# Kernel optimization log

Measured on AMD Instinct MI355X. Metric: run time of the kernel, lower is better.

Reference implementation:

```python
import jax, jax.numpy as jnp
import numpy as np

IN_F = 512
OUT_F = 512
TREES = 50
DEPTH = 10  # levels above leaves; 2^DEPTH leaves per tree


def _build_forest(T, D):
    """Forest of T perfect binary trees. Nodes laid out level-by-level (leaves first).
    Returns node_order [N], adjacency [E,2] (parent, child; children consecutive,
    left then right, edges sorted by parent), edge_order [E]."""
    per = 2 ** (D + 1) - 1
    no = np.zeros(per, np.int64)
    adj_parts, eo_parts = [], []
    start, prev = 0, None
    for l in range(D + 1):
        n_l = 2 ** (D - l)
        idx = np.arange(start, start + n_l, dtype=np.int64)
        no[idx] = l
        if l > 0:
            parents = np.repeat(idx, 2)          # each parent twice
            adj_parts.append(np.stack([parents, prev], 1))  # prev = 2*n_l children, pairs consecutive
            eo_parts.append(np.full(2 * n_l, l, np.int64))
        prev, start = idx, start + n_l
    adj = np.concatenate(adj_parts, 0)
    eo = np.concatenate(eo_parts, 0)
    offs = np.arange(T, dtype=np.int64) * per
    node_order = np.tile(no, T)
    adjacency = (adj[None] + offs[:, None, None]).reshape(-1, 2)
    edge_order = np.tile(eo, T)
    return node_order, adjacency, edge_order


def setup_inputs() -> dict:
    key = jax.random.key(0)
    ks = jax.random.split(key, 8)
    no, adj, eo = _build_forest(TREES, DEPTH)
    N = no.shape[0]
    s_in = 1.0 / np.sqrt(IN_F).astype(np.float32)
    s_h = 1.0 / np.sqrt(OUT_F).astype(np.float32)
    return {
        "features": jax.random.normal(ks[0], (N, IN_F), jnp.float32),
        "node_order": jnp.asarray(no),
        "adjacency_list": jnp.asarray(adj),
        "edge_order": jnp.asarray(eo),
        "W_iou_w": jax.random.normal(ks[1], (3 * OUT_F, IN_F), jnp.float32) * s_in,
        "W_iou_b": jax.random.normal(ks[2], (3 * OUT_F,), jnp.float32) * s_in,
        "U_iou_l": jax.random.normal(ks[3], (3 * OUT_F, OUT_F), jnp.float32) * s_h,
        "U_iou_r": jax.random.normal(ks[4], (3 * OUT_F, OUT_F), jnp.float32) * s_h,
        "W_f_w": jax.random.normal(ks[5], (OUT_F, IN_F), jnp.float32) * s_in,
        "W_f_b": jax.random.normal(ks[6], (OUT_F,), jnp.float32) * s_in,
        "U_f_l": jax.random.normal(ks[7], (OUT_F, OUT_F), jnp.float32) * s_h,
        "U_f_r": jax.random.normal(jax.random.fold_in(key, 99), (OUT_F, OUT_F), jnp.float32) * s_h,
    }


def reference(features, node_order, adjacency_list, edge_order,
              W_iou_w, W_iou_b, U_iou_l, U_iou_r, W_f_w, W_f_b, U_f_l, U_f_r):
    # Tree topology is static integer data: hoist it to numpy so per-level index
    # sets are concrete (the original torch code host-syncs the same way).
    no = np.asarray(node_order)
    ao = np.asarray(adjacency_list)
    eo = np.asarray(edge_order)
    N, H = features.shape[0], W_f_w.shape[0]
    h = jnp.zeros((N, H), features.dtype)
    c = jnp.zeros((N, H), features.dtype)
    for l in range(int(no.max()) + 1):
        nodes = jnp.asarray(np.nonzero(no == l)[0])   # parents at this level, sorted
        x = features[nodes]                            # [P, F]
        if l == 0:
            iou = x @ W_iou_w.T + W_iou_b
            i, o, u = jnp.split(iou, 3, axis=1)
            c_new = jax.nn.sigmoid(i) * jnp.tanh(u)
        else:
            e = ao[eo == l]                            # [2P, 2]; children consecutive per parent
            p_rep = jnp.asarray(e[:, 0])               # parent repeated per child
            children = jnp.asarray(e[:, 1])
            ch = h[children]                           # [2P, H]
            cc = c[children]                           # [2P, H]
            iou = (x @ W_iou_w.T + W_iou_b
                   + ch[0::2] @ U_iou_l.T              # left child h
                   + ch[1::2] @ U_iou_r.T)             # right child h
            i, o, u = jnp.split(iou, 3, axis=1)
            wf = features[p_rep] @ W_f_w.T + W_f_b     # [2P, H]
            f_l = jax.nn.sigmoid(wf + ch @ U_f_l.T)
            f_r = jax.nn.sigmoid(wf + ch @ U_f_r.T)
            fc = (f_l + f_r) * cc                      # [2P, H]
            c_new = jax.nn.sigmoid(i) * jnp.tanh(u) + fc.reshape(-1, 2, H).sum(1)
        h_new = jax.nn.sigmoid(o) * jnp.tanh(c_new)
        c = c.at[nodes].set(c_new)
        h = h.at[nodes].set(h_new)
    return h, c
```

## Files before the change

kernel.cpp:

```cpp
#include <hip/hip_runtime.h>
#include <hip/hip_bf16.h>

#define TREES_ 50
#define PER_ 2047
#define NN_ (TREES_ * PER_)
#define NINT_ (TREES_ * 1023)
#define NLEAF_ (TREES_ * 1024)

typedef __attribute__((ext_vector_type(8))) short s8v;
typedef __attribute__((ext_vector_type(4))) float f4v;

__device__ __forceinline__ unsigned short f2bf(float f) {
  union { float f; unsigned u; } v; v.f = f;
  unsigned r = v.u + 0x7FFFu + ((v.u >> 16) & 1u);
  return (unsigned short)(r >> 16);
}
__device__ __forceinline__ float bf2f(unsigned short s) {
  union { unsigned u; float f; } v; v.u = ((unsigned)s) << 16;
  return v.f;
}
__device__ __forceinline__ float sigm(float x) { return 1.f / (1.f + __expf(-x)); }
__device__ __forceinline__ float tanh_s(float x) {
  float ax = fabsf(x);
  float e = __expf(2.f * ax);
  float t = 1.f - 2.f / (e + 1.f);
  return copysignf(t, x);
}
__device__ __forceinline__ f4v fz4() { f4v z; z[0]=0.f; z[1]=0.f; z[2]=0.f; z[3]=0.f; return z; }

#if defined(__has_builtin)
#if __has_builtin(__builtin_amdgcn_global_load_lds)
#define HAS_GLD 1
#endif
#endif
__device__ __forceinline__ void gld16(const void* g, void* l) {
#ifdef HAS_GLD
  __builtin_amdgcn_global_load_lds(
      (const __attribute__((address_space(1))) unsigned int*)g,
      (__attribute__((address_space(3))) unsigned int*)l, 16, 0, 0);
#else
  *(s8v*)l = *(const s8v*)g;
#endif
}

__device__ __forceinline__ int xcd_swz(int bid, int nwg) {
  int q = nwg >> 3, r = nwg & 7, x = bid & 7, pos = bid >> 3;
  int base = (x < r) ? x * (q + 1) : r * (q + 1) + (x - r) * q;
  return base + pos;
}

#define LDS_BYTE(row, c16) ((row) * 128 + (((c16) ^ ((row) & 7)) << 4))

#define MFMA_STEP(Ap, Bp)                                                     \
  _Pragma("unroll") for (int kk = 0; kk < 2; ++kk) {                          \
    s8v af[4], bf_[4];                                                        \
    _Pragma("unroll") for (int i = 0; i < 4; ++i) {                           \
      int R = wr * 64 + i * 16 + lr;                                          \
      af[i] = *(const s8v*)((const char*)(Ap) + LDS_BYTE(R, kk * 4 + lg));    \
    }                                                                         \
    _Pragma("unroll") for (int j = 0; j < 4; ++j) {                           \
      int R = wc * 64 + j * 16 + lr;                                          \
      bf_[j] = *(const s8v*)((const char*)(Bp) + LDS_BYTE(R, kk * 4 + lg));   \
    }                                                                         \
    _Pragma("unroll") for (int i = 0; i < 4; ++i)                             \
      _Pragma("unroll") for (int j = 0; j < 4; ++j)                           \
        acc[i][j] = __builtin_amdgcn_mfma_f32_16x16x32_bf16(af[i], bf_[j],    \
                                                            acc[i][j], 0, 0, 0); \
  }

#define VMCNT8() asm volatile("s_waitcnt vmcnt(8)" ::: "memory")
#define VMCNT0() asm volatile("s_waitcnt vmcnt(0)" ::: "memory")
#define LGKM0()  asm volatile("s_waitcnt lgkmcnt(0)" ::: "memory")
#define SBAR()   __builtin_amdgcn_s_barrier()
#define SCHEDB() __builtin_amdgcn_sched_barrier(0)

#define PIPELINE(STAGEM, NT)                                       \
  STAGEM(0, 0)                                                     \
  STAGEM(1, 64)                                                    \
  {                                                                \
    int cur = 0;                                                   \
    for (int t = 0; t < (NT) - 1; ++t) {                           \
      VMCNT8(); SBAR();                                            \
      __builtin_amdgcn_s_setprio(1);                               \
      MFMA_STEP(AsB + cur * 8192, BsB + cur * 8192)                \
      __builtin_amdgcn_s_setprio(0);                               \
      LGKM0(); SCHEDB(); SBAR();                                   \
      if (t + 2 < (NT)) { STAGEM(cur, (t + 2) * 64) }              \
      cur ^= 1;                                                    \
    }                                                              \
    VMCNT0(); SBAR();                                              \
    MFMA_STEP(AsB + cur * 8192, BsB + cur * 8192)                  \
  }

__global__ __launch_bounds__(256) void feat2bf(const float* __restrict__ feat,
                                               unsigned short* __restrict__ FB) {
  long long i = (long long)blockIdx.x * 256 + threadIdx.x;
  if (i >= (long long)NN_ * 64) return;
  const float* src = feat + i * 8;
  float4 f0 = *(const float4*)src;
  float4 f1 = *(const float4*)(src + 4);
  s8v v;
  v[0] = (short)f2bf(f0.x); v[1] = (short)f2bf(f0.y);
  v[2] = (short)f2bf(f0.z); v[3] = (short)f2bf(f0.w);
  v[4] = (short)f2bf(f1.x); v[5] = (short)f2bf(f1.y);
  v[6] = (short)f2bf(f1.z); v[7] = (short)f2bf(f1.w);
  *(s8v*)(FB + i * 8) = v;
}

__global__ __launch_bounds__(256) void prep_weights(
    const float* __restrict__ Wiou, const float* __restrict__ Ul,
    const float* __restrict__ Ur,  const float* __restrict__ Wf,
    const float* __restrict__ Ufl, const float* __restrict__ Ufr,
    unsigned short* __restrict__ UCAT2, unsigned short* __restrict__ UFLR,
    unsigned short* __restrict__ WFB) {
  int i = blockIdx.x * 256 + threadIdx.x;
  if (i < 1536 * 1536) {
    int r = i / 1536, c = i - r * 1536;
    float v = (c < 512) ? Ul[r * 512 + c]
            : (c < 1024) ? Ur[r * 512 + (c - 512)]
                         : Wiou[r * 512 + (c - 1024)];
    UCAT2[i] = f2bf(v);
  }
  if (i < 1024 * 512) {
    int r = i >> 9, k = i & 511;
    int c = r >> 1, s = r & 1;
    UFLR[i] = f2bf(s ? Ufr[c * 512 + k] : Ufl[c * 512 + k]);
  }
  if (i < 512 * 512) WFB[i] = f2bf(Wf[i]);
}

__global__ __launch_bounds__(256) void pre_mm(
    const unsigned short* __restrict__ FB, const unsigned short* __restrict__ WFB,
    const unsigned short* __restrict__ UCAT2,
    const float* __restrict__ bfb, const float* __restrict__ biou,
    unsigned short* __restrict__ WF, unsigned short* __restrict__ LIOU,
    int nwgW, int nwgL) {
  __shared__ __align__(16) unsigned short AsB[2 * 128 * 64];
  __shared__ __align__(16) unsigned short BsB[2 * 128 * 64];
  const int tid = threadIdx.x;
  const int wid = tid >> 6, lane = tid & 63;
  const int wr = wid >> 1, wc = wid & 1;
  const int lr = lane & 15, lg = lane >> 4;
  f4v acc[4][4];
#pragma unroll
  for (int i = 0; i < 4; ++i)
#pragma unroll
    for (int j = 0; j < 4; ++j) acc[i][j] = fz4();

  const unsigned short* aA[4]; const unsigned short* aB[4];
  int tm, tn;
  const bool isW = (int)blockIdx.x < nwgW;
  if (isW) {
    const int swz = xcd_swz(blockIdx.x, nwgW);
    tn = swz & 3; tm = swz >> 2;
#pragma unroll
    for (int L = 0; L < 4; ++L) {
      int q = L * 256 + tid;
      int row = q >> 3, c16g = (q & 7) ^ (row & 7);
      int m = tm * 128 + row; if (m >= NINT_) m = NINT_ - 1;
      unsigned t = (unsigned)m / 1023u;
      int node = (int)t * 2047 + 1024 + (m - (int)t * 1023);
      aA[L] = FB + (size_t)node * 512 + c16g * 8;
      int n = tn * 128 + row;
      aB[L] = WFB + (size_t)n * 512 + c16g * 8;
    }
  } else {
    const int swz = xcd_swz((int)blockIdx.x - nwgW, nwgL);
    tn = swz % 12; tm = swz / 12;
#pragma unroll
    for (int L = 0; L < 4; ++L) {
      int q = L * 256 + tid;
      int row = q >> 3, c16g = (q & 7) ^ (row & 7);
      int m = tm * 128 + row;
      int node = (m >> 10) * 2047 + (m & 1023);
      aA[L] = FB + (size_t)node * 512 + c16g * 8;
      int n = tn * 128 + row;
      aB[L] = UCAT2 + (size_t)n * 1536 + 1024 + c16g * 8;
    }
  }
#define STAGE_P(bb, kofs)                                         \
  _Pragma("unroll") for (int L = 0; L < 4; ++L) {                 \
    int q = L * 256 + tid;                                        \
    gld16(aA[L] + (kofs), AsB + (bb) * 8192 + q * 8);             \
    gld16(aB[L] + (kofs), BsB + (bb) * 8192 + q * 8);             \
  }
  PIPELINE(STAGE_P, 8)

  if (isW) {
#pragma unroll
    for (int i = 0; i < 4; ++i)
#pragma unroll
      for (int j = 0; j < 4; ++j) {
        int n = tn * 128 + wc * 64 + j * 16 + lr;
        float bias = bfb[n];
#pragma unroll
        for (int r = 0; r < 4; ++r) {
          int m = tm * 128 + wr * 64 + i * 16 + lg * 4 + r;
          if (m < NINT_) WF[(size_t)m * 512 + n] = f2bf(acc[i][j][r] + bias);
        }
      }
  } else {
#pragma unroll
    for (int i = 0; i < 4; ++i)
#pragma unroll
      for (int j = 0; j < 4; ++j) {
        int n = tn * 128 + wc * 64 + j * 16 + lr;
        float bias = biou[n];
#pragma unroll
        for (int r = 0; r < 4; ++r) {
          int m = tm * 128 + wr * 64 + i * 16 + lg * 4 + r;
          LIOU[(size_t)m * 1536 + n] = f2bf(acc[i][j][r] + bias);
        }
      }
  }
}

__global__ __launch_bounds__(256) void leaf_ew(
    const unsigned short* __restrict__ LIOU,
    float* __restrict__ h_out, float* __restrict__ c_out,
    unsigned short* __restrict__ HB) {
  int idx = blockIdx.x * 256 + threadIdx.x;
  int r = idx >> 7;
  int c4 = (idx & 127) << 2;
  int g = (r >> 10) * 2047 + (r & 1023);
  const unsigned short* pr = LIOU + (size_t)r * 1536;
  ushort4 iv = *(const ushort4*)(pr + c4);
  ushort4 ov = *(const ushort4*)(pr + 512 + c4);
  ushort4 uv = *(const ushort4*)(pr + 1024 + c4);
  float4 hv, cv; ushort4 hb;
  float cc, hh;
  cc = sigm(bf2f(iv.x)) * tanh_s(bf2f(uv.x)); hh = sigm(bf2f(ov.x)) * tanh_s(cc);
  cv.x = cc; hv.x = hh; hb.x = f2bf(hh);
  cc = sigm(bf2f(iv.y)) * tanh_s(bf2f(uv.y)); hh = sigm(bf2f(ov.y)) * tanh_s(cc);
  cv.y = cc; hv.y = hh; hb.y = f2bf(hh);
  cc = sigm(bf2f(iv.z)) * tanh_s(bf2f(uv.z)); hh = sigm(bf2f(ov.z)) * tanh_s(cc);
  cv.z = cc; hv.z = hh; hb.z = f2bf(hh);
  cc = sigm(bf2f(iv.w)) * tanh_s(bf2f(uv.w)); hh = sigm(bf2f(ov.w)) * tanh_s(cc);
  cv.w = cc; hv.w = hh; hb.w = f2bf(hh);
  *(float4*)(h_out + (size_t)g * 512 + c4) = hv;
  *(float4*)(c_out + (size_t)g * 512 + c4) = cv;
  *(ushort4*)(HB + (size_t)g * 512 + c4) = hb;
}

__global__ __launch_bounds__(256) void lvl_gemm(
    const unsigned short* __restrict__ HB, const unsigned short* __restrict__ FB,
    const unsigned short* __restrict__ UFLR, const unsigned short* __restrict__ UCAT2,
    const unsigned short* __restrict__ WF, const float* __restrict__ biou,
    const float* __restrict__ c_out, float* __restrict__ h_out,
    unsigned short* __restrict__ IOU,
    int P, int shift, int start_l, int start_lm1, int nwg1, int nwg2) {
  __shared__ __align__(16) unsigned short AsB[2 * 128 * 64];
  __shared__ __align__(16) unsigned short BsB[2 * 128 * 64];
  const int tid = threadIdx.x;
  const int wid = tid >> 6, lane = tid & 63;
  const int wr = wid >> 1, wc = wid & 1;
  const int lr = lane & 15, lg = lane >> 4;
  const int pmask = (1 << shift) - 1;
  f4v acc[4][4];
#pragma unroll
  for (int i = 0; i < 4; ++i)
#pragma unroll
    for (int j = 0; j < 4; ++j) acc[i][j] = fz4();

  if ((int)blockIdx.x < nwg1) {
    const int swz = xcd_swz(blockIdx.x, nwg1);
    const int tn = swz & 7, tm = swz >> 3;
    const int M2 = 2 * P;
    const int cmask = (2 << shift) - 1;
    const unsigned short* aA[4]; const unsigned short* aB[4];
#pragma unroll
    for (int L = 0; L < 4; ++L) {
      int q = L * 256 + tid;
      int row = q >> 3, c16g = (q & 7) ^ (row & 7);
      int jg = tm * 128 + row; if (jg >= M2) jg = M2 - 1;
      int t = jg >> (shift + 1), idx = jg & cmask;
      aA[L] = HB + (size_t)(t * PER_ + start_lm1 + idx) * 512 + c16g * 8;
      int n = tn * 128 + row;
      aB[L] = UFLR + (size_t)n * 512 + c16g * 8;
    }
#define STAGE_G1(bb, kofs)                                        \
  _Pragma("unroll") for (int L = 0; L < 4; ++L) {                 \
    int q = L * 256 + tid;                                        \
    gld16(aA[L] + (kofs), AsB + (bb) * 8192 + q * 8);             \
    gld16(aB[L] + (kofs), BsB + (bb) * 8192 + q * 8);             \
  }
    PIPELINE(STAGE_G1, 8)

    const int soff = start_l - 1024;
#pragma unroll
    for (int i = 0; i < 4; ++i) {
      int mbase = tm * 128 + wr * 64 + i * 16;
#pragma unroll
      for (int j = 0; j < 4; ++j) {
        int nn = tn * 128 + wc * 64 + j * 16 + lr;
        int hcol = nn >> 1;
        float fc[4];
#pragma unroll
        for (int r = 0; r < 4; ++r) {
          int m = mbase + lg * 4 + r;
          int mm = (m < M2) ? m : 0;
          int pidx = mm >> 1;
          int t = pidx >> shift, k = pidx & pmask;
          float wf = bf2f(WF[(size_t)(t * 1023 + soff + k) * 512 + hcol]);
          float sv = sigm(wf + acc[i][j][r]);
          float spair = sv + __shfl_xor(sv, 1, 64);
          float cc = 0.f;
          if ((lr & 1) == 0)
            cc = c_out[(size_t)(t * PER_ + start_lm1 + (mm & cmask)) * 512 + hcol];
          fc[r] = spair * cc;
        }
        if ((lr & 1) == 0) {
          int p0 = (mbase >> 1) + lg * 2;
          if (p0 < P) {
            int t0 = p0 >> shift, k0p = p0 & pmask;
            h_out[(size_t)(t0 * PER_ + start_l + k0p) * 512 + hcol] = fc[0] + fc[1];
          }
          int p1 = (mbase >> 1) + lg * 2 + 1;
          if (p1 < P) {
            int t1 = p1 >> shift, k1p = p1 & pmask;
            h_out[(size_t)(t1 * PER_ + start_l + k1p) * 512 + hcol] = fc[2] + fc[3];
          }
        }
      }
    }
  } else {
    const int swz = xcd_swz((int)blockIdx.x - nwg1, nwg2);
    const int tn = swz % 12, tm = swz / 12;
    const unsigned short* aHB[4]; const unsigned short* aFB[4];
    const unsigned short* aB[4];
#pragma unroll
    for (int L = 0; L < 4; ++L) {
      int q = L * 256 + tid;
      int row = q >> 3, c16g = (q & 7) ^ (row & 7);
      int p = tm * 128 + row; if (p >= P) p = P - 1;
      int t = p >> shift, kp = p & pmask;
      aHB[L] = HB + (size_t)(t * PER_ + start_lm1) * 512 + (size_t)kp * 1024 + c16g * 8;
      aFB[L] = FB + (size_t)(t * PER_ + start_l + kp) * 512 + c16g * 8 - 1024;
      int n = tn * 128 + row;
      aB[L] = UCAT2 + (size_t)n * 1536 + c16g * 8;
    }
#define STAGE_G2(bb, kofs)                                                    \
  _Pragma("unroll") for (int L = 0; L < 4; ++L) {                             \
    int q = L * 256 + tid;                                                    \
    const unsigned short* srcA =                                              \
        ((kofs) < 1024) ? aHB[L] + (kofs) : aFB[L] + (kofs);                  \
    gld16(srcA, AsB + (bb) * 8192 + q * 8);                                   \
    gld16(aB[L] + (kofs), BsB + (bb) * 8192 + q * 8);                         \
  }
    PIPELINE(STAGE_G2, 24)
#pragma unroll
    for (int i = 0; i < 4; ++i)
#pragma unroll
      for (int j = 0; j < 4; ++j) {
        int n = tn * 128 + wc * 64 + j * 16 + lr;
        float bias = biou[n];
#pragma unroll
        for (int r = 0; r < 4; ++r) {
          int m = tm * 128 + wr * 64 + i * 16 + lg * 4 + r;
          if (m < P) IOU[(size_t)m * 1536 + n] = f2bf(acc[i][j][r] + bias);
        }
      }
  }
}

__global__ __launch_bounds__(256) void g3_kernel(
    const unsigned short* __restrict__ IOU,
    float* __restrict__ h_out, float* __restrict__ c_out,
    unsigned short* __restrict__ HB, int P, int shift, int start_l) {
  int idx = blockIdx.x * 256 + threadIdx.x;
  int p = idx >> 7;
  if (p >= P) return;
  int c4 = (idx & 127) << 2;
  int t = p >> shift, k = p & ((1 << shift) - 1);
  size_t pg = (size_t)(t * PER_ + start_l + k);
  const unsigned short* ir = IOU + (size_t)p * 1536;
  ushort4 iv = *(const ushort4*)(ir + c4);
  ushort4 ov = *(const ushort4*)(ir + 512 + c4);
  ushort4 uv = *(const ushort4*)(ir + 1024 + c4);
  float4 fcs = *(const float4*)(h_out + pg * 512 + c4);
  float4 hv, cv; ushort4 hb;
  float cc, hh;
  cc = sigm(bf2f(iv.x)) * tanh_s(bf2f(uv.x)) + fcs.x; hh = sigm(bf2f(ov.x)) * tanh_s(cc);
  cv.x = cc; hv.x = hh; hb.x = f2bf(hh);
  cc = sigm(bf2f(iv.y)) * tanh_s(bf2f(uv.y)) + fcs.y; hh = sigm(bf2f(ov.y)) * tanh_s(cc);
  cv.y = cc; hv.y = hh; hb.y = f2bf(hh);
  cc = sigm(bf2f(iv.z)) * tanh_s(bf2f(uv.z)) + fcs.z; hh = sigm(bf2f(ov.z)) * tanh_s(cc);
  cv.z = cc; hv.z = hh; hb.z = f2bf(hh);
  cc = sigm(bf2f(iv.w)) * tanh_s(bf2f(uv.w)) + fcs.w; hh = sigm(bf2f(ov.w)) * tanh_s(cc);
  cv.w = cc; hv.w = hh; hb.w = f2bf(hh);
  *(float4*)(h_out + pg * 512 + c4) = hv;
  *(float4*)(c_out + pg * 512 + c4) = cv;
  *(ushort4*)(HB + pg * 512 + c4) = hb;
}

__global__ void fill_sentinel(float* out, int n) {
  int i = blockIdx.x * 256 + threadIdx.x;
  if (i < n) out[i] = 12345.0f;
}

extern "C" void kernel_launch(void* const* d_in, const int* in_sizes, int n_in,
                              void* d_out, int out_size, void* d_ws, size_t ws_size,
                              hipStream_t stream) {
  (void)in_sizes; (void)n_in; (void)out_size;
  const float* feat = (const float*)d_in[0];
  const float* Wiou = (const float*)d_in[4];
  const float* biou = (const float*)d_in[5];
  const float* Ul   = (const float*)d_in[6];
  const float* Ur   = (const float*)d_in[7];
  const float* Wf   = (const float*)d_in[8];
  const float* bfb  = (const float*)d_in[9];
  const float* Ufl  = (const float*)d_in[10];
  const float* Ufr  = (const float*)d_in[11];
  float* h_out = (float*)d_out;
  float* c_out = h_out + (size_t)NN_ * 512;

  const size_t OFF_HB   = 0;
  const size_t SZ_HB    = (size_t)NN_ * 512 * 2;
  const size_t OFF_FB   = OFF_HB + SZ_HB;
  const size_t SZ_FB    = (size_t)NN_ * 512 * 2;
  const size_t OFF_WFm  = OFF_FB + SZ_FB;
  const size_t SZ_WF    = (size_t)NINT_ * 512 * 2;
  const size_t OFF_UC2  = OFF_WFm + SZ_WF;
  const size_t SZ_UC2   = 1536 * 1536 * 2;
  const size_t OFF_UFLR = OFF_UC2 + SZ_UC2;
  const size_t SZ_UFLR  = 1024 * 512 * 2;
  const size_t OFF_WFB  = OFF_UFLR + SZ_UFLR;
  const size_t SZ_WFB   = 512 * 512 * 2;
  const size_t OFF_LIOU = OFF_WFB + SZ_WFB;
  const size_t SZ_LIOU  = (size_t)NLEAF_ * 1536 * 2;
  const size_t NEEDED   = OFF_LIOU + SZ_LIOU;

  if (ws_size < NEEDED) {
    int n = 2 * NN_ * 512;
    fill_sentinel<<<(n + 255) / 256, 256, 0, stream>>>((float*)d_out, n);
    return;
  }

  char* ws = (char*)d_ws;
  unsigned short* HB    = (unsigned short*)(ws + OFF_HB);
  unsigned short* FB    = (unsigned short*)(ws + OFF_FB);
  unsigned short* WF    = (unsigned short*)(ws + OFF_WFm);
  unsigned short* UCAT2 = (unsigned short*)(ws + OFF_UC2);
  unsigned short* UFLR  = (unsigned short*)(ws + OFF_UFLR);
  unsigned short* WFB   = (unsigned short*)(ws + OFF_WFB);
  unsigned short* LIOU  = (unsigned short*)(ws + OFF_LIOU);
  unsigned short* IOU   = (unsigned short*)(ws + OFF_LIOU);

  prep_weights<<<9216, 256, 0, stream>>>(Wiou, Ul, Ur, Wf, Ufl, Ufr,
                                         UCAT2, UFLR, WFB);
  feat2bf<<<(NN_ * 64 + 255) / 256, 256, 0, stream>>>(feat, FB);
  {
    int nwgW = ((NINT_ + 127) / 128) * 4;
    int nwgL = (NLEAF_ / 128) * 12;
    pre_mm<<<nwgW + nwgL, 256, 0, stream>>>(FB, WFB, UCAT2, bfb, biou,
                                            WF, LIOU, nwgW, nwgL);
  }
  leaf_ew<<<(NLEAF_ * 128) / 256, 256, 0, stream>>>(LIOU, h_out, c_out, HB);

  for (int l = 1; l <= 10; ++l) {
    int shift = 10 - l;
    int P = TREES_ << shift;
    int start_l   = 2048 - (1 << (11 - l));
    int start_lm1 = 2048 - (1 << (12 - l));
    int nwg1 = ((2 * P + 127) / 128) * 8;
    int nwg2 = ((P + 127) / 128) * 12;
    lvl_gemm<<<nwg1 + nwg2, 256, 0, stream>>>(HB, FB, UFLR, UCAT2, WF, biou,
                                              c_out, h_out, IOU,
                                              P, shift, start_l, start_lm1,
                                              nwg1, nwg2);
    int g3b = (P * 128 + 255) / 256;
    g3_kernel<<<g3b, 256, 0, stream>>>(IOU, h_out, c_out, HB, P, shift, start_l);
  }
}
```

Before: 1.460 ms.

## Fuse leaf IOU GEMM with leaf elementwise gates, drop LIOU buffer

```diff
diff --git a/kernel.cpp b/kernel.cpp
--- a/kernel.cpp
+++ b/kernel.cpp
@@ -129,117 +129,126 @@
   if (i < 512 * 512) WFB[i] = f2bf(Wf[i]);
 }
 
-__global__ __launch_bounds__(256) void pre_mm(
+__global__ __launch_bounds__(256) void wf_gemm(
     const unsigned short* __restrict__ FB, const unsigned short* __restrict__ WFB,
-    const unsigned short* __restrict__ UCAT2,
-    const float* __restrict__ bfb, const float* __restrict__ biou,
-    unsigned short* __restrict__ WF, unsigned short* __restrict__ LIOU,
-    int nwgW, int nwgL) {
+    const float* __restrict__ bfb, unsigned short* __restrict__ WF, int nwg) {
   __shared__ __align__(16) unsigned short AsB[2 * 128 * 64];
   __shared__ __align__(16) unsigned short BsB[2 * 128 * 64];
   const int tid = threadIdx.x;
+  const int swz = xcd_swz(blockIdx.x, nwg);
+  const int tn = swz & 3, tm = swz >> 2;
   const int wid = tid >> 6, lane = tid & 63;
   const int wr = wid >> 1, wc = wid & 1;
   const int lr = lane & 15, lg = lane >> 4;
+  const unsigned short* aA[4]; const unsigned short* aB[4];
+#pragma unroll
+  for (int L = 0; L < 4; ++L) {
+    int q = L * 256 + tid;
+    int row = q >> 3, c16g = (q & 7) ^ (row & 7);
+    int m = tm * 128 + row; if (m >= NINT_) m = NINT_ - 1;
+    int t = (int)((unsigned)m / 1023u);
+    int node = t * 2047 + 1024 + (m - t * 1023);
+    aA[L] = FB + (size_t)node * 512 + c16g * 8;
+    int n = tn * 128 + row;
+    aB[L] = WFB + (size_t)n * 512 + c16g * 8;
+  }
   f4v acc[4][4];
 #pragma unroll
   for (int i = 0; i < 4; ++i)
 #pragma unroll
     for (int j = 0; j < 4; ++j) acc[i][j] = fz4();
-
-  const unsigned short* aA[4]; const unsigned short* aB[4];
-  int tm, tn;
-  const bool isW = (int)blockIdx.x < nwgW;
-  if (isW) {
-    const int swz = xcd_swz(blockIdx.x, nwgW);
-    tn = swz & 3; tm = swz >> 2;
-#pragma unroll
-    for (int L = 0; L < 4; ++L) {
-      int q = L * 256 + tid;
-      int row = q >> 3, c16g = (q & 7) ^ (row & 7);
-      int m = tm * 128 + row; if (m >= NINT_) m = NINT_ - 1;
-      unsigned t = (unsigned)m / 1023u;
-      int node = (int)t * 2047 + 1024 + (m - (int)t * 1023);
-      aA[L] = FB + (size_t)node * 512 + c16g * 8;
-      int n = tn * 128 + row;
-      aB[L] = WFB + (size_t)n * 512 + c16g * 8;
-    }
-  } else {
-    const int swz = xcd_swz((int)blockIdx.x - nwgW, nwgL);
-    tn = swz % 12; tm = swz / 12;
-#pragma unroll
-    for (int L = 0; L < 4; ++L) {
-      int q = L * 256 + tid;
-      int row = q >> 3, c16g = (q & 7) ^ (row & 7);
-      int m = tm * 128 + row;
-      int node = (m >> 10) * 2047 + (m & 1023);
-      aA[L] = FB + (size_t)node * 512 + c16g * 8;
-      int n = tn * 128 + row;
-      aB[L] = UCAT2 + (size_t)n * 1536 + 1024 + c16g * 8;
-    }
-  }
-#define STAGE_P(bb, kofs)                                         \
+#define STAGE_W(bb, kofs)                                         \
   _Pragma("unroll") for (int L = 0; L < 4; ++L) {                 \
     int q = L * 256 + tid;                                        \
     gld16(aA[L] + (kofs), AsB + (bb) * 8192 + q * 8);             \
     gld16(aB[L] + (kofs), BsB + (bb) * 8192 + q * 8);             \
   }
-  PIPELINE(STAGE_P, 8)
-
-  if (isW) {
+  PIPELINE(STAGE_W, 8)
+#pragma unroll
+  for (int i = 0; i < 4; ++i)
+#pragma unroll
+    for (int j = 0; j < 4; ++j) {
+      int n = tn * 128 + wc * 64 + j * 16 + lr;
+      float bias = bfb[n];
+#pragma unroll
+      for (int r = 0; r < 4; ++r) {
+        int m = tm * 128 + wr * 64 + i * 16 + lg * 4 + r;
+        if (m < NINT_) WF[(size_t)m * 512 + n] = f2bf(acc[i][j][r] + bias);
+      }
+    }
+}
+
+__global__ __launch_bounds__(256) void leaf_mm(
+    const unsigned short* __restrict__ FB, const unsigned short* __restrict__ UCAT2,
+    const float* __restrict__ biou,
+    float* __restrict__ h_out, float* __restrict__ c_out,
+    unsigned short* __restrict__ HB, int nwg) {
+  __shared__ __align__(16) unsigned short As[128 * 64];
+  __shared__ __align__(16) unsigned short Bs[128 * 64];
+  const int tid = threadIdx.x;
+  const int swz = xcd_swz(blockIdx.x, nwg);
+  const int cs = swz & 3, tm = swz >> 2;
+  const int wid = tid >> 6, lane = tid & 63;
+  const int wr = wid >> 1, wc = wid & 1;
+  const int lr = lane & 15, lg = lane >> 4;
+  const unsigned short* aA[4]; const unsigned short* aB0[4];
+#pragma unroll
+  for (int L = 0; L < 4; ++L) {
+    int q = L * 256 + tid;
+    int row = q >> 3, c16g = (q & 7) ^ (row & 7);
+    int m = tm * 128 + row;
+    int node = (m >> 10) * 2047 + (m & 1023);
+    aA[L] = FB + (size_t)node * 512 + c16g * 8;
+    aB0[L] = UCAT2 + (size_t)(cs * 128 + row) * 1536 + 1024 + c16g * 8;
+  }
+  f4v sv[4][4];
+  const int goff[3] = {0, 1024, 512};
+#pragma unroll
+  for (int gg = 0; gg < 3; ++gg) {
+    const size_t boff = (size_t)goff[gg] * 1536;
+    f4v acc[4][4];
 #pragma unroll
     for (int i = 0; i < 4; ++i)
 #pragma unroll
+      for (int j = 0; j < 4; ++j) acc[i][j] = fz4();
+    for (int k0 = 0; k0 < 512; k0 += 64) {
+#pragma unroll
+      for (int L = 0; L < 4; ++L) {
+        int q = L * 256 + tid;
+        gld16(aA[L] + k0, (unsigned short*)As + q * 8);
+        gld16(aB0[L] + boff + k0, (unsigned short*)Bs + q * 8);
+      }
+      __syncthreads();
+      MFMA_STEP(As, Bs)
+      __syncthreads();
+    }
+#pragma unroll
+    for (int i = 0; i < 4; ++i)
+#pragma unroll
       for (int j = 0; j < 4; ++j) {
-        int n = tn * 128 + wc * 64 + j * 16 + lr;
-        float bias = bfb[n];
+        int coln = cs * 128 + wc * 64 + j * 16 + lr;
+        float bias = biou[goff[gg] + coln];
 #pragma unroll
         for (int r = 0; r < 4; ++r) {
-          int m = tm * 128 + wr * 64 + i * 16 + lg * 4 + r;
-          if (m < NINT_) WF[(size_t)m * 512 + n] = f2bf(acc[i][j][r] + bias);
+          float v = acc[i][j][r] + bias;
+          if (gg == 0) {
+            sv[i][j][r] = sigm(v);
+          } else if (gg == 1) {
+            float cvv = sv[i][j][r] * tanh_s(v);
+            sv[i][j][r] = cvv;
+            int m = tm * 128 + wr * 64 + i * 16 + lg * 4 + r;
+            int node = (m >> 10) * 2047 + (m & 1023);
+            c_out[(size_t)node * 512 + coln] = cvv;
+          } else {
+            float hh = sigm(v) * tanh_s(sv[i][j][r]);
+            int m = tm * 128 + wr * 64 + i * 16 + lg * 4 + r;
+            int node = (m >> 10) * 2047 + (m & 1023);
+            h_out[(size_t)node * 512 + coln] = hh;
+            HB[(size_t)node * 512 + coln] = f2bf(hh);
+          }
         }
       }
-  } else {
-#pragma unroll
-    for (int i = 0; i < 4; ++i)
-#pragma unroll
-      for (int j = 0; j < 4; ++j) {
-        int n = tn * 128 + wc * 64 + j * 16 + lr;
-        float bias = biou[n];
-#pragma unroll
-        for (int r = 0; r < 4; ++r) {
-          int m = tm * 128 + wr * 64 + i * 16 + lg * 4 + r;
-          LIOU[(size_t)m * 1536 + n] = f2bf(acc[i][j][r] + bias);
-        }
-      }
-  }
-}
-
-__global__ __launch_bounds__(256) void leaf_ew(
-    const unsigned short* __restrict__ LIOU,
-    float* __restrict__ h_out, float* __restrict__ c_out,
-    unsigned short* __restrict__ HB) {
-  int idx = blockIdx.x * 256 + threadIdx.x;
-  int r = idx >> 7;
-  int c4 = (idx & 127) << 2;
-  int g = (r >> 10) * 2047 + (r & 1023);
-  const unsigned short* pr = LIOU + (size_t)r * 1536;
-  ushort4 iv = *(const ushort4*)(pr + c4);
-  ushort4 ov = *(const ushort4*)(pr + 512 + c4);
-  ushort4 uv = *(const ushort4*)(pr + 1024 + c4);
-  float4 hv, cv; ushort4 hb;
-  float cc, hh;
-  cc = sigm(bf2f(iv.x)) * tanh_s(bf2f(uv.x)); hh = sigm(bf2f(ov.x)) * tanh_s(cc);
-  cv.x = cc; hv.x = hh; hb.x = f2bf(hh);
-  cc = sigm(bf2f(iv.y)) * tanh_s(bf2f(uv.y)); hh = sigm(bf2f(ov.y)) * tanh_s(cc);
-  cv.y = cc; hv.y = hh; hb.y = f2bf(hh);
-  cc = sigm(bf2f(iv.z)) * tanh_s(bf2f(uv.z)); hh = sigm(bf2f(ov.z)) * tanh_s(cc);
-  cv.z = cc; hv.z = hh; hb.z = f2bf(hh);
-  cc = sigm(bf2f(iv.w)) * tanh_s(bf2f(uv.w)); hh = sigm(bf2f(ov.w)) * tanh_s(cc);
-  cv.w = cc; hv.w = hh; hb.w = f2bf(hh);
-  *(float4*)(h_out + (size_t)g * 512 + c4) = hv;
-  *(float4*)(c_out + (size_t)g * 512 + c4) = cv;
-  *(ushort4*)(HB + (size_t)g * 512 + c4) = hb;
+  }
 }
 
 __global__ __launch_bounds__(256) void lvl_gemm(
@@ -426,9 +435,9 @@
   const size_t SZ_UFLR  = 1024 * 512 * 2;
   const size_t OFF_WFB  = OFF_UFLR + SZ_UFLR;
   const size_t SZ_WFB   = 512 * 512 * 2;
-  const size_t OFF_LIOU = OFF_WFB + SZ_WFB;
-  const size_t SZ_LIOU  = (size_t)NLEAF_ * 1536 * 2;
-  const size_t NEEDED   = OFF_LIOU + SZ_LIOU;
+  const size_t OFF_IOU  = OFF_WFB + SZ_WFB;
+  const size_t SZ_IOU   = (size_t)25600 * 1536 * 2;
+  const size_t NEEDED   = OFF_IOU + SZ_IOU;
 
   if (ws_size < NEEDED) {
     int n = 2 * NN_ * 512;
@@ -443,19 +452,19 @@
   unsigned short* UCAT2 = (unsigned short*)(ws + OFF_UC2);
   unsigned short* UFLR  = (unsigned short*)(ws + OFF_UFLR);
   unsigned short* WFB   = (unsigned short*)(ws + OFF_WFB);
-  unsigned short* LIOU  = (unsigned short*)(ws + OFF_LIOU);
-  unsigned short* IOU   = (unsigned short*)(ws + OFF_LIOU);
+  unsigned short* IOU   = (unsigned short*)(ws + OFF_IOU);
 
   prep_weights<<<9216, 256, 0, stream>>>(Wiou, Ul, Ur, Wf, Ufl, Ufr,
                                          UCAT2, UFLR, WFB);
   feat2bf<<<(NN_ * 64 + 255) / 256, 256, 0, stream>>>(feat, FB);
   {
     int nwgW = ((NINT_ + 127) / 128) * 4;
-    int nwgL = (NLEAF_ / 128) * 12;
-    pre_mm<<<nwgW + nwgL, 256, 0, stream>>>(FB, WFB, UCAT2, bfb, biou,
-                                            WF, LIOU, nwgW, nwgL);
-  }
-  leaf_ew<<<(NLEAF_ * 128) / 256, 256, 0, stream>>>(LIOU, h_out, c_out, HB);
+    wf_gemm<<<nwgW, 256, 0, stream>>>(FB, WFB, bfb, WF, nwgW);
+  }
+  {
+    int nwgL = (NLEAF_ / 128) * 4;
+    leaf_mm<<<nwgL, 256, 0, stream>>>(FB, UCAT2, biou, h_out, c_out, HB, nwgL);
+  }
 
   for (int l = 1; l <= 10; ++l) {
     int shift = 10 - l;
```

After: 1.699 ms. 16.4% more time.

## Fuse forget-gate GEMM into IOU GEMM per level, reusing child-h tiles

Applied to the files above, without the earlier changes.

```diff
diff --git a/kernel.cpp b/kernel.cpp
--- a/kernel.cpp
+++ b/kernel.cpp
@@ -41,6 +41,11 @@
 #else
   *(s8v*)l = *(const s8v*)g;
 #endif
+}
+__device__ __forceinline__ s8v gload16(const void* p) {
+  s8v r;
+  asm volatile("global_load_dwordx4 %0, %1, off" : "=v"(r) : "v"(p) : "memory");
+  return r;
 }
 
 __device__ __forceinline__ int xcd_swz(int bid, int nwg) {
@@ -129,12 +134,60 @@
   if (i < 512 * 512) WFB[i] = f2bf(Wf[i]);
 }
 
+__global__ __launch_bounds__(256) void wf_gemm(
+    const unsigned short* __restrict__ FB, const unsigned short* __restrict__ WFB,
+    const float* __restrict__ bfb, unsigned short* __restrict__ WF, int nwg) {
+  __shared__ __align__(16) unsigned short AsB[2 * 128 * 64];
+  __shared__ __align__(16) unsigned short BsB[2 * 128 * 64];
+  const int tid = threadIdx.x;
+  const int swz = xcd_swz(blockIdx.x, nwg);
+  const int tn = swz & 3, tm = swz >> 2;
+  const int wid = tid >> 6, lane = tid & 63;
+  const int wr = wid >> 1, wc = wid & 1;
+  const int lr = lane & 15, lg = lane >> 4;
+  const unsigned short* aA[4]; const unsigned short* aB[4];
+#pragma unroll
+  for (int L = 0; L < 4; ++L) {
+    int q = L * 256 + tid;
+    int row = q >> 3, c16g = (q & 7) ^ (row & 7);
+    int m = tm * 128 + row; if (m >= NINT_) m = NINT_ - 1;
+    int t = (int)((unsigned)m / 1023u);
+    int node = t * 2047 + 1024 + (m - t * 1023);
+    aA[L] = FB + (size_t)node * 512 + c16g * 8;
+    int n = tn * 128 + row;
+    aB[L] = WFB + (size_t)n * 512 + c16g * 8;
+  }
+  f4v acc[4][4];
+#pragma unroll
+  for (int i = 0; i < 4; ++i)
+#pragma unroll
+    for (int j = 0; j < 4; ++j) acc[i][j] = fz4();
+#define STAGE_W(bb, kofs)                                         \
+  _Pragma("unroll") for (int L = 0; L < 4; ++L) {                 \
+    int q = L * 256 + tid;                                        \
+    gld16(aA[L] + (kofs), AsB + (bb) * 8192 + q * 8);             \
+    gld16(aB[L] + (kofs), BsB + (bb) * 8192 + q * 8);             \
+  }
+  PIPELINE(STAGE_W, 8)
+#pragma unroll
+  for (int i = 0; i < 4; ++i)
+#pragma unroll
+    for (int j = 0; j < 4; ++j) {
+      int n = tn * 128 + wc * 64 + j * 16 + lr;
+      float bias = bfb[n];
+#pragma unroll
+      for (int r = 0; r < 4; ++r) {
+        int m = tm * 128 + wr * 64 + i * 16 + lg * 4 + r;
+        if (m < NINT_) WF[(size_t)m * 512 + n] = f2bf(acc[i][j][r] + bias);
+      }
+    }
+}
+
 __global__ __launch_bounds__(256) void pre_mm(
-    const unsigned short* __restrict__ FB, const unsigned short* __restrict__ WFB,
+    const unsigned short* __restrict__ FB,
     const unsigned short* __restrict__ UCAT2,
-    const float* __restrict__ bfb, const float* __restrict__ biou,
-    unsigned short* __restrict__ WF, unsigned short* __restrict__ LIOU,
-    int nwgW, int nwgL) {
+    const float* __restrict__ biou,
+    unsigned short* __restrict__ LIOU, int nwg) {
   __shared__ __align__(16) unsigned short AsB[2 * 128 * 64];
   __shared__ __align__(16) unsigned short BsB[2 * 128 * 64];
   const int tid = threadIdx.x;
@@ -146,37 +199,18 @@
   for (int i = 0; i < 4; ++i)
 #pragma unroll
     for (int j = 0; j < 4; ++j) acc[i][j] = fz4();
-
   const unsigned short* aA[4]; const unsigned short* aB[4];
-  int tm, tn;
-  const bool isW = (int)blockIdx.x < nwgW;
-  if (isW) {
-    const int swz = xcd_swz(blockIdx.x, nwgW);
-    tn = swz & 3; tm = swz >> 2;
-#pragma unroll
-    for (int L = 0; L < 4; ++L) {
-      int q = L * 256 + tid;
-      int row = q >> 3, c16g = (q & 7) ^ (row & 7);
-      int m = tm * 128 + row; if (m >= NINT_) m = NINT_ - 1;
-      unsigned t = (unsigned)m / 1023u;
-      int node = (int)t * 2047 + 1024 + (m - (int)t * 1023);
-      aA[L] = FB + (size_t)node * 512 + c16g * 8;
-      int n = tn * 128 + row;
-      aB[L] = WFB + (size_t)n * 512 + c16g * 8;
-    }
-  } else {
-    const int swz = xcd_swz((int)blockIdx.x - nwgW, nwgL);
-    tn = swz % 12; tm = swz / 12;
-#pragma unroll
-    for (int L = 0; L < 4; ++L) {
-      int q = L * 256 + tid;
-      int row = q >> 3, c16g = (q & 7) ^ (row & 7);
-      int m = tm * 128 + row;
-      int node = (m >> 10) * 2047 + (m & 1023);
-      aA[L] = FB + (size_t)node * 512 + c16g * 8;
-      int n = tn * 128 + row;
-      aB[L] = UCAT2 + (size_t)n * 1536 + 1024 + c16g * 8;
-    }
+  const int swz = xcd_swz(blockIdx.x, nwg);
+  const int tn = swz % 12, tm = swz / 12;
+#pragma unroll
+  for (int L = 0; L < 4; ++L) {
+    int q = L * 256 + tid;
+    int row = q >> 3, c16g = (q & 7) ^ (row & 7);
+    int m = tm * 128 + row;
+    int node = (m >> 10) * 2047 + (m & 1023);
+    aA[L] = FB + (size_t)node * 512 + c16g * 8;
+    int n = tn * 128 + row;
+    aB[L] = UCAT2 + (size_t)n * 1536 + 1024 + c16g * 8;
   }
 #define STAGE_P(bb, kofs)                                         \
   _Pragma("unroll") for (int L = 0; L < 4; ++L) {                 \
@@ -185,34 +219,18 @@
     gld16(aB[L] + (kofs), BsB + (bb) * 8192 + q * 8);             \
   }
   PIPELINE(STAGE_P, 8)
-
-  if (isW) {
-#pragma unroll
-    for (int i = 0; i < 4; ++i)
-#pragma unroll
-      for (int j = 0; j < 4; ++j) {
-        int n = tn * 128 + wc * 64 + j * 16 + lr;
-        float bias = bfb[n];
-#pragma unroll
-        for (int r = 0; r < 4; ++r) {
-          int m = tm * 128 + wr * 64 + i * 16 + lg * 4 + r;
-          if (m < NINT_) WF[(size_t)m * 512 + n] = f2bf(acc[i][j][r] + bias);
-        }
-      }
-  } else {
-#pragma unroll
-    for (int i = 0; i < 4; ++i)
-#pragma unroll
-      for (int j = 0; j < 4; ++j) {
-        int n = tn * 128 + wc * 64 + j * 16 + lr;
-        float bias = biou[n];
-#pragma unroll
-        for (int r = 0; r < 4; ++r) {
-          int m = tm * 128 + wr * 64 + i * 16 + lg * 4 + r;
-          LIOU[(size_t)m * 1536 + n] = f2bf(acc[i][j][r] + bias);
-        }
-      }
-  }
+#pragma unroll
+  for (int i = 0; i < 4; ++i)
+#pragma unroll
+    for (int j = 0; j < 4; ++j) {
+      int n = tn * 128 + wc * 64 + j * 16 + lr;
+      float bias = biou[n];
+#pragma unroll
+      for (int r = 0; r < 4; ++r) {
+        int m = tm * 128 + wr * 64 + i * 16 + lg * 4 + r;
+        LIOU[(size_t)m * 1536 + n] = f2bf(acc[i][j][r] + bias);
+      }
+    }
 }
 
 __global__ __launch_bounds__(256) void leaf_ew(
@@ -242,13 +260,13 @@
   *(ushort4*)(HB + (size_t)g * 512 + c4) = hb;
 }
 
-__global__ __launch_bounds__(256) void lvl_gemm(
+__global__ __launch_bounds__(256, 2) void lvl_fused(
     const unsigned short* __restrict__ HB, const unsigned short* __restrict__ FB,
     const unsigned short* __restrict__ UFLR, const unsigned short* __restrict__ UCAT2,
     const unsigned short* __restrict__ WF, const float* __restrict__ biou,
     const float* __restrict__ c_out, float* __restrict__ h_out,
     unsigned short* __restrict__ IOU,
-    int P, int shift, int start_l, int start_lm1, int nwg1, int nwg2) {
+    int P, int shift, int start_l, int start_lm1, int nwg) {
   __shared__ __align__(16) unsigned short AsB[2 * 128 * 64];
   __shared__ __align__(16) unsigned short BsB[2 * 128 * 64];
   const int tid = threadIdx.x;
@@ -256,90 +274,36 @@
   const int wr = wid >> 1, wc = wid & 1;
   const int lr = lane & 15, lg = lane >> 4;
   const int pmask = (1 << shift) - 1;
+  const int swz = xcd_swz(blockIdx.x, nwg);
+  const int tn = swz % 12, tm = swz / 12;
+  const bool doG1 = (tn < 8);
+  const int soff = start_l - 1024;
+
   f4v acc[4][4];
+  f4v accG1[4][4];
 #pragma unroll
   for (int i = 0; i < 4; ++i)
 #pragma unroll
-    for (int j = 0; j < 4; ++j) acc[i][j] = fz4();
-
-  if ((int)blockIdx.x < nwg1) {
-    const int swz = xcd_swz(blockIdx.x, nwg1);
-    const int tn = swz & 7, tm = swz >> 3;
-    const int M2 = 2 * P;
-    const int cmask = (2 << shift) - 1;
-    const unsigned short* aA[4]; const unsigned short* aB[4];
-#pragma unroll
-    for (int L = 0; L < 4; ++L) {
-      int q = L * 256 + tid;
-      int row = q >> 3, c16g = (q & 7) ^ (row & 7);
-      int jg = tm * 128 + row; if (jg >= M2) jg = M2 - 1;
-      int t = jg >> (shift + 1), idx = jg & cmask;
-      aA[L] = HB + (size_t)(t * PER_ + start_lm1 + idx) * 512 + c16g * 8;
-      int n = tn * 128 + row;
-      aB[L] = UFLR + (size_t)n * 512 + c16g * 8;
-    }
-#define STAGE_G1(bb, kofs)                                        \
-  _Pragma("unroll") for (int L = 0; L < 4; ++L) {                 \
-    int q = L * 256 + tid;                                        \
-    gld16(aA[L] + (kofs), AsB + (bb) * 8192 + q * 8);             \
-    gld16(aB[L] + (kofs), BsB + (bb) * 8192 + q * 8);             \
-  }
-    PIPELINE(STAGE_G1, 8)
-
-    const int soff = start_l - 1024;
-#pragma unroll
-    for (int i = 0; i < 4; ++i) {
-      int mbase = tm * 128 + wr * 64 + i * 16;
-#pragma unroll
-      for (int j = 0; j < 4; ++j) {
-        int nn = tn * 128 + wc * 64 + j * 16 + lr;
-        int hcol = nn >> 1;
-        float fc[4];
-#pragma unroll
-        for (int r = 0; r < 4; ++r) {
-          int m = mbase + lg * 4 + r;
-          int mm = (m < M2) ? m : 0;
-          int pidx = mm >> 1;
-          int t = pidx >> shift, k = pidx & pmask;
-          float wf = bf2f(WF[(size_t)(t * 1023 + soff + k) * 512 + hcol]);
-          float sv = sigm(wf + acc[i][j][r]);
-          float spair = sv + __shfl_xor(sv, 1, 64);
-          float cc = 0.f;
-          if ((lr & 1) == 0)
-            cc = c_out[(size_t)(t * PER_ + start_lm1 + (mm & cmask)) * 512 + hcol];
-          fc[r] = spair * cc;
-        }
-        if ((lr & 1) == 0) {
-          int p0 = (mbase >> 1) + lg * 2;
-          if (p0 < P) {
-            int t0 = p0 >> shift, k0p = p0 & pmask;
-            h_out[(size_t)(t0 * PER_ + start_l + k0p) * 512 + hcol] = fc[0] + fc[1];
-          }
-          int p1 = (mbase >> 1) + lg * 2 + 1;
-          if (p1 < P) {
-            int t1 = p1 >> shift, k1p = p1 & pmask;
-            h_out[(size_t)(t1 * PER_ + start_l + k1p) * 512 + hcol] = fc[2] + fc[3];
-          }
-        }
-      }
-    }
-  } else {
-    const int swz = xcd_swz((int)blockIdx.x - nwg1, nwg2);
-    const int tn = swz % 12, tm = swz / 12;
-    const unsigned short* aHB[4]; const unsigned short* aFB[4];
-    const unsigned short* aB[4];
-#pragma unroll
-    for (int L = 0; L < 4; ++L) {
-      int q = L * 256 + tid;
-      int row = q >> 3, c16g = (q & 7) ^ (row & 7);
-      int p = tm * 128 + row; if (p >= P) p = P - 1;
-      int t = p >> shift, kp = p & pmask;
-      aHB[L] = HB + (size_t)(t * PER_ + start_lm1) * 512 + (size_t)kp * 1024 + c16g * 8;
-      aFB[L] = FB + (size_t)(t * PER_ + start_l + kp) * 512 + c16g * 8 - 1024;
-      int n = tn * 128 + row;
-      aB[L] = UCAT2 + (size_t)n * 1536 + c16g * 8;
-    }
-#define STAGE_G2(bb, kofs)                                                    \
+    for (int j = 0; j < 4; ++j) { acc[i][j] = fz4(); accG1[i][j] = fz4(); }
+
+  const unsigned short* aHB[4]; const unsigned short* aFB[4];
+  const unsigned short* aB[4];
+#pragma unroll
+  for (int L = 0; L < 4; ++L) {
+    int q = L * 256 + tid;
+    int row = q >> 3, c16g = (q & 7) ^ (row & 7);
+    int p = tm * 128 + row; if (p >= P) p = P - 1;
+    int t = p >> shift, kp = p & pmask;
+    aHB[L] = HB + (size_t)(t * PER_ + start_lm1) * 512 + (size_t)kp * 1024 + c16g * 8;
+    aFB[L] = FB + (size_t)(t * PER_ + start_l + kp) * 512 + c16g * 8 - 1024;
+    int n = tn * 128 + row;
+    aB[L] = UCAT2 + (size_t)n * 1536 + c16g * 8;
+  }
+  const unsigned short* ub =
+      UFLR + (size_t)(tn * 128 + wc * 64 + lr) * 512 + lg * 8;
+  s8v breg[8];
+
+#define STAGE_F(bb, kofs)                                                     \
   _Pragma("unroll") for (int L = 0; L < 4; ++L) {                             \
     int q = L * 256 + tid;                                                    \
     const unsigned short* srcA =                                              \
@@ -347,20 +311,100 @@
     gld16(srcA, AsB + (bb) * 8192 + q * 8);                                   \
     gld16(aB[L] + (kofs), BsB + (bb) * 8192 + q * 8);                         \
   }
-    PIPELINE(STAGE_G2, 24)
-#pragma unroll
-    for (int i = 0; i < 4; ++i)
+#define BREGLOAD(tc)                                                          \
+  {                                                                           \
+    int kw = ((tc) & 7) * 64;                                                 \
+    _Pragma("unroll") for (int h = 0; h < 2; ++h)                             \
+    _Pragma("unroll") for (int j = 0; j < 4; ++j)                             \
+      breg[h * 4 + j] = gload16(ub + (size_t)j * 8192 + kw + h * 32);         \
+  }
+#define G1_EPI(S)                                                             \
+  _Pragma("unroll") for (int i = 0; i < 4; ++i)                               \
+  _Pragma("unroll") for (int j = 0; j < 4; ++j) {                             \
+    int n = tn * 128 + wc * 64 + j * 16 + lr;                                 \
+    int hcol = n >> 1;                                                        \
+    _Pragma("unroll") for (int r = 0; r < 4; ++r) {                           \
+      int p = tm * 128 + wr * 64 + i * 16 + lg * 4 + r;                       \
+      int pc = (p < P) ? p : 0;                                               \
+      int t_ = pc >> shift, k_ = pc & pmask;                                  \
+      size_t mi = (size_t)(t_ * 1023 + soff + k_);                            \
+      float wf = bf2f(WF[mi * 512 + hcol]);                                   \
+      float sv = sigm(wf + accG1[i][j][r]);                                   \
+      float sp = sv + __shfl_xor(sv, 1, 64);                                  \
+      if (((lr & 1) == 0) && (p < P)) {                                       \
+        size_t cg = (size_t)(t_ * PER_ + start_lm1 + 2 * k_ + (S));           \
+        float fc = sp * c_out[cg * 512 + hcol];                               \
+        size_t pp = (size_t)(t_ * PER_ + start_l + k_) * 512 + hcol;          \
+        if ((S) == 0) h_out[pp] = fc; else h_out[pp] += fc;                   \
+      }                                                                       \
+    }                                                                         \
+  }
+
+  if (doG1) BREGLOAD(0)
+  STAGE_F(0, 0)
+  STAGE_F(1, 64)
+  int cur = 0;
+  for (int t = 0; t < 24; ++t) {
+    if (t < 23) { VMCNT8(); } else { VMCNT0(); }
+    SCHEDB(); SBAR();
+    __builtin_amdgcn_s_setprio(1);
+#pragma unroll
+    for (int kk = 0; kk < 2; ++kk) {
+      s8v af[4], bf_[4];
+#pragma unroll
+      for (int i = 0; i < 4; ++i) {
+        int R = wr * 64 + i * 16 + lr;
+        af[i] = *(const s8v*)((const char*)(AsB + cur * 8192) + LDS_BYTE(R, kk * 4 + lg));
+      }
 #pragma unroll
       for (int j = 0; j < 4; ++j) {
-        int n = tn * 128 + wc * 64 + j * 16 + lr;
-        float bias = biou[n];
-#pragma unroll
-        for (int r = 0; r < 4; ++r) {
-          int m = tm * 128 + wr * 64 + i * 16 + lg * 4 + r;
-          if (m < P) IOU[(size_t)m * 1536 + n] = f2bf(acc[i][j][r] + bias);
-        }
-      }
-  }
+        int R = wc * 64 + j * 16 + lr;
+        bf_[j] = *(const s8v*)((const char*)(BsB + cur * 8192) + LDS_BYTE(R, kk * 4 + lg));
+      }
+#pragma unroll
+      for (int i = 0; i < 4; ++i)
+#pragma unroll
+        for (int j = 0; j < 4; ++j)
+          acc[i][j] = __builtin_amdgcn_mfma_f32_16x16x32_bf16(af[i], bf_[j], acc[i][j], 0, 0, 0);
+      if (doG1 && t < 16) {
+#pragma unroll
+        for (int i = 0; i < 4; ++i)
+#pragma unroll
+          for (int j = 0; j < 4; ++j)
+            accG1[i][j] = __builtin_amdgcn_mfma_f32_16x16x32_bf16(
+                af[i], breg[kk * 4 + j], accG1[i][j], 0, 0, 0);
+      }
+    }
+    __builtin_amdgcn_s_setprio(0);
+    LGKM0(); SCHEDB(); SBAR();
+    if (doG1) {
+      if (t == 7) {
+        G1_EPI(0)
+#pragma unroll
+        for (int i = 0; i < 4; ++i)
+#pragma unroll
+          for (int j = 0; j < 4; ++j) accG1[i][j] = fz4();
+      } else if (t == 15) {
+        G1_EPI(1)
+      }
+      if (t + 1 < 16) BREGLOAD(t + 1)
+    }
+    if (t + 2 < 24) { STAGE_F(cur, (t + 2) * 64) }
+    cur ^= 1;
+  }
+
+#pragma unroll
+  for (int i = 0; i < 4; ++i)
+#pragma unroll
+    for (int j = 0; j < 4; ++j) {
+      int n = tn * 128 + wc * 64 + j * 16 + lr;
+      float bias = biou[n];
+#pragma unroll
+      for (int r = 0; r < 4; ++r) {
+        int m = tm * 128 + wr * 64 + i * 16 + lg * 4 + r;
+        if (m < P) IOU[(size_t)m * 1536 + n] = f2bf(acc[i][j][r] + bias);
+      }
+    }
 }
 
 __global__ __launch_bounds__(256) void g3_kernel(
@@ -451,9 +495,11 @@
   feat2bf<<<(NN_ * 64 + 255) / 256, 256, 0, stream>>>(feat, FB);
   {
     int nwgW = ((NINT_ + 127) / 128) * 4;
+    wf_gemm<<<nwgW, 256, 0, stream>>>(FB, WFB, bfb, WF, nwgW);
+  }
+  {
     int nwgL = (NLEAF_ / 128) * 12;
-    pre_mm<<<nwgW + nwgL, 256, 0, stream>>>(FB, WFB, UCAT2, bfb, biou,
-                                            WF, LIOU, nwgW, nwgL);
+    pre_mm<<<nwgL, 256, 0, stream>>>(FB, UCAT2, biou, LIOU, nwgL);
   }
   leaf_ew<<<(NLEAF_ * 128) / 256, 256, 0, stream>>>(LIOU, h_out, c_out, HB);
 
@@ -462,12 +508,10 @@
     int P = TREES_ << shift;
     int start_l   = 2048 - (1 << (11 - l));
     int start_lm1 = 2048 - (1 << (12 - l));
-    int nwg1 = ((2 * P + 127) / 128) * 8;
-    int nwg2 = ((P + 127) / 128) * 12;
-    lvl_gemm<<<nwg1 + nwg2, 256, 0, stream>>>(HB, FB, UFLR, UCAT2, WF, biou,
-                                              c_out, h_out, IOU,
-                                              P, shift, start_l, start_lm1,
-                                              nwg1, nwg2);
+    int nwg = ((P + 127) / 128) * 12;
+    lvl_fused<<<nwg, 256, 0, stream>>>(HB, FB, UFLR, UCAT2, WF, biou,
+                                       c_out, h_out, IOU,
+                                       P, shift, start_l, start_lm1, nwg);
     int g3b = (P * 128 + 255) / 256;
     g3_kernel<<<g3b, 256, 0, stream>>>(IOU, h_out, c_out, HB, P, shift, start_l);
   }
```

After: 3.164 ms. 2.17x slower.
